# Kernel tuning notes

Hardware: AMD Instinct MI355X
Metric: run time of the kernel (lower is better)

The kernel has to match this reference:

```python
import jax, jax.numpy as jnp
import numpy as np
import math

B, S, N_EMBD, HEAD_SIZE = 32, 2048, 64, 64

def setup_inputs() -> dict:
    key = jax.random.key(0)
    k1, k2, k3, k4 = jax.random.split(key, 4)
    inputs = jax.random.normal(k1, (B, S, N_EMBD), dtype=jnp.float32)
    # nn.Linear(n_embd, head_size, bias=False) weights: shape (head_size, n_embd)
    scale = 1.0 / math.sqrt(N_EMBD)
    Wq = jax.random.normal(k2, (HEAD_SIZE, N_EMBD), dtype=jnp.float32) * scale
    Wk = jax.random.normal(k3, (HEAD_SIZE, N_EMBD), dtype=jnp.float32) * scale
    Wv = jax.random.normal(k4, (HEAD_SIZE, N_EMBD), dtype=jnp.float32) * scale
    return {"inputs": inputs, "Wq": Wq, "Wk": Wk, "Wv": Wv}

def reference(inputs, Wq, Wk, Wv):
    # q, k, v: [B, S, head_size]
    q = jnp.einsum('bse,he->bsh', inputs, Wq)
    k = jnp.einsum('bse,he->bsh', inputs, Wk)
    v = jnp.einsum('bse,he->bsh', inputs, Wv)
    scores = jnp.einsum('bqh,bkh->bqk', q, k) / jnp.sqrt(jnp.float32(HEAD_SIZE))
    # NOTE: the original torch code calls scores.masked_fill(...) out-of-place
    # and discards the result, so NO causal mask is actually applied.
    attention = jax.nn.softmax(scores, axis=-1)
    out = jnp.einsum('bqk,bkh->bqh', attention, v)  # [B, S, head_size]
    return out
```

## Files before the change

kernel.cpp:

```cpp
#include <hip/hip_runtime.h>


#define BATCH 32
#define SEQ   2048
#define HS    64
#define QSCALE 0.18033688011112042f
#define OTS   72
#define OPAD  20

typedef _Float16 f16x8 __attribute__((ext_vector_type(8)));
typedef _Float16 f16x4 __attribute__((ext_vector_type(4)));
typedef float    f32x4 __attribute__((ext_vector_type(4)));

__global__ __launch_bounds__(256) void prep_w(
    const float* __restrict__ Wq, const float* __restrict__ Wk,
    const float* __restrict__ Wv, _Float16* __restrict__ Wh)
{
    int i = blockIdx.x * 256 + threadIdx.x;
    int rep = i / 12288;
    int j = i - rep * 12288;
    const float* src = (j < 4096) ? Wq : ((j < 8192) ? Wk : Wv);
    float scale = (j < 4096) ? QSCALE : 1.0f;
    Wh[i] = (_Float16)(src[j & 4095] * scale);
}

__global__ __launch_bounds__(256) void proj_kernel(
    const float* __restrict__ x, const _Float16* __restrict__ Wh,
    _Float16* __restrict__ Qh, _Float16* __restrict__ Kh,
    _Float16* __restrict__ Vt)
{
    __shared__ __align__(16) _Float16 ot[64 * OTS];

    const int t    = threadIdx.x;
    const int w    = t >> 6;
    const int lane = t & 63;
    const int lo   = lane & 15;
    const int quad = lane >> 4;
    const long blk0 = (long)blockIdx.x * 64;
    const int  b    = (int)(blk0 / SEQ);
    const int  s0   = (int)(blk0 % SEQ);
    const long rw   = blk0 + w * 16;
    const _Float16* Wrep = Wh + (blockIdx.x & 7) * 12288;

    const float* xp = x + (rw + lo) * HS + quad * 8;
    float4 x0 = *(const float4*)xp;
    float4 x1 = *(const float4*)(xp + 4);
    float4 x2 = *(const float4*)(xp + 32);
    float4 x3 = *(const float4*)(xp + 36);
    f16x8 xb0, xb1;
    xb0[0]=(_Float16)x0.x; xb0[1]=(_Float16)x0.y; xb0[2]=(_Float16)x0.z; xb0[3]=(_Float16)x0.w;
    xb0[4]=(_Float16)x1.x; xb0[5]=(_Float16)x1.y; xb0[6]=(_Float16)x1.z; xb0[7]=(_Float16)x1.w;
    xb1[0]=(_Float16)x2.x; xb1[1]=(_Float16)x2.y; xb1[2]=(_Float16)x2.z; xb1[3]=(_Float16)x2.w;
    xb1[4]=(_Float16)x3.x; xb1[5]=(_Float16)x3.y; xb1[6]=(_Float16)x3.z; xb1[7]=(_Float16)x3.w;

#pragma unroll
    for (int m = 0; m < 3; ++m) {
        const _Float16* Wm = Wrep + m * 4096;
        f32x4 acc[4];
#pragma unroll
        for (int nt = 0; nt < 4; ++nt) { acc[nt][0]=0.f; acc[nt][1]=0.f; acc[nt][2]=0.f; acc[nt][3]=0.f; }
#pragma unroll
        for (int nt = 0; nt < 4; ++nt) {
            f16x8 wa0 = *(const f16x8*)(Wm + (nt * 16 + lo) * 64 + quad * 8);
            f16x8 wa1 = *(const f16x8*)(Wm + (nt * 16 + lo) * 64 + 32 + quad * 8);
            acc[nt] = __builtin_amdgcn_mfma_f32_16x16x32_f16(wa0, xb0, acc[nt], 0, 0, 0);
            acc[nt] = __builtin_amdgcn_mfma_f32_16x16x32_f16(wa1, xb1, acc[nt], 0, 0, 0);
        }
        if (m < 2) {
            _Float16* dst = (m == 0) ? Qh : Kh;
#pragma unroll
            for (int nt = 0; nt < 4; ++nt) {
                f16x4 pk;
                pk[0]=(_Float16)acc[nt][0]; pk[1]=(_Float16)acc[nt][1];
                pk[2]=(_Float16)acc[nt][2]; pk[3]=(_Float16)acc[nt][3];
                *(f16x4*)(dst + (rw + lo) * HS + nt * 16 + quad * 4) = pk;
            }
        } else {
#pragma unroll
            for (int nt = 0; nt < 4; ++nt)
#pragma unroll
                for (int r = 0; r < 4; ++r)
                    ot[(nt * 16 + quad * 4 + r) * OTS + w * 16 + lo] = (_Float16)acc[nt][r];
            __syncthreads();
            const int row = t >> 2, c = t & 3;
            f16x8 r0 = *(const f16x8*)(ot + row * OTS + c * 16);
            f16x8 r1 = *(const f16x8*)(ot + row * OTS + c * 16 + 8);
            _Float16* vd = Vt + ((long)b * HS + row) * SEQ + s0 + c * 16;
            *(f16x8*)vd       = r0;
            *(f16x8*)(vd + 8) = r1;
        }
    }
}

__global__ __launch_bounds__(256) void attn_kernel(
    const _Float16* __restrict__ Q, const _Float16* __restrict__ K,
    const _Float16* __restrict__ Vt, float* __restrict__ out)
{
    __shared__ __align__(16) _Float16 KV[2][8192];

    const int t    = threadIdx.x;
    const int w    = t >> 6;
    const int lane = t & 63;
    const int lo   = lane & 15;
    const int quad = lane >> 4;
    const int sr   = t >> 2, sc = t & 3;
    const int xr   = lo & 7;

    const int bid = blockIdx.x;
    const int b   = (bid & 7) | ((bid >> 8) << 3);
    const int qt  = (bid >> 3) & 31;
    const int q0  = qt * 64;
    const int qh  = w >> 1;
    const int kh  = w & 1;

    const _Float16* Qb = Q + ((long)b * SEQ + q0 + qh * 32) * HS;
    f16x8 qf[2][2];
#pragma unroll
    for (int q2 = 0; q2 < 2; ++q2) {
        qf[q2][0] = *(const f16x8*)(Qb + (q2 * 16 + lo) * HS + quad * 8);
        qf[q2][1] = *(const f16x8*)(Qb + (q2 * 16 + lo) * HS + 32 + quad * 8);
    }

    const _Float16* Kb = K  + (long)b * SEQ * HS;
    const _Float16* Vb = Vt + (long)b * HS * SEQ;

    const int pr  = (sr & 32) | ((sr & 4) << 2) | ((sr & 24) >> 1) | (sr & 3);
    const int kw0 = pr * 64 + (((2 * sc    ) ^ (pr & 7)) << 3);
    const int kw1 = pr * 64 + (((2 * sc + 1) ^ (pr & 7)) << 3);
    const int vw0 = 4096 + sr * 64 + (((2 * sc    ) ^ (sr & 7)) << 3);
    const int vw1 = 4096 + sr * 64 + (((2 * sc + 1) ^ (sr & 7)) << 3);

    const int kr0 = (kh * 32      + lo) * 64;
    const int kr1 = (kh * 32 + 16 + lo) * 64;
    const int g0  = ((quad    ) ^ xr) << 3;
    const int g1  = ((4 + quad) ^ xr) << 3;
    int voff[4];
#pragma unroll
    for (int ht = 0; ht < 4; ++ht)
        voff[ht] = 4096 + (ht * 16 + lo) * 64 + (((kh * 4 + quad) ^ xr) << 3);

    f32x4 o[2][4], ol[2];
#pragma unroll
    for (int q2 = 0; q2 < 2; ++q2) {
        ol[q2][0]=0.f; ol[q2][1]=0.f; ol[q2][2]=0.f; ol[q2][3]=0.f;
#pragma unroll
        for (int ht = 0; ht < 4; ++ht) { o[q2][ht][0]=0.f; o[q2][ht][1]=0.f; o[q2][ht][2]=0.f; o[q2][ht][3]=0.f; }
    }
    f32x4 zz; zz[0]=0.f; zz[1]=0.f; zz[2]=0.f; zz[3]=0.f;
    f16x8 ones;
#pragma unroll
    for (int j = 0; j < 8; ++j) ones[j] = (_Float16)1.0f;

    const int key0 = (qt & 31) << 6;
    f16x8 kfA = *(const f16x8*)(Kb + (long)(key0 + sr) * HS + sc * 16);
    f16x8 kfB = *(const f16x8*)(Kb + (long)(key0 + sr) * HS + sc * 16 + 8);
    f16x8 vfA = *(const f16x8*)(Vb + (long)sr * SEQ + key0 + sc * 16);
    f16x8 vfB = *(const f16x8*)(Vb + (long)sr * SEQ + key0 + sc * 16 + 8);

    for (int kt = 0; kt < 32; ++kt) {
        _Float16* Ksp = &KV[kt & 1][0];
        *(f16x8*)(Ksp + kw0) = kfA;
        *(f16x8*)(Ksp + kw1) = kfB;
        *(f16x8*)(Ksp + vw0) = vfA;
        *(f16x8*)(Ksp + vw1) = vfB;

        const int keyn = ((kt + 1 + qt) & 31) << 6;
        kfA = *(const f16x8*)(Kb + (long)(keyn + sr) * HS + sc * 16);
        kfB = *(const f16x8*)(Kb + (long)(keyn + sr) * HS + sc * 16 + 8);
        vfA = *(const f16x8*)(Vb + (long)sr * SEQ + keyn + sc * 16);
        vfB = *(const f16x8*)(Vb + (long)sr * SEQ + keyn + sc * 16 + 8);

        __syncthreads();

        f16x8 ka00 = *(const f16x8*)(Ksp + kr0 + g0);
        f16x8 ka01 = *(const f16x8*)(Ksp + kr0 + g1);
        f16x8 ka10 = *(const f16x8*)(Ksp + kr1 + g0);
        f16x8 ka11 = *(const f16x8*)(Ksp + kr1 + g1);

        f16x8 vbf[4];
#pragma unroll
        for (int ht = 0; ht < 4; ++ht)
            vbf[ht] = *(const f16x8*)(Ksp + voff[ht]);

#pragma unroll
        for (int q2 = 0; q2 < 2; ++q2) {
            f32x4 s0, s1;
            s0 = __builtin_amdgcn_mfma_f32_16x16x32_f16(ka00, qf[q2][0], zz, 0, 0, 0);
            s0 = __builtin_amdgcn_mfma_f32_16x16x32_f16(ka01, qf[q2][1], s0, 0, 0, 0);
            s1 = __builtin_amdgcn_mfma_f32_16x16x32_f16(ka10, qf[q2][0], zz, 0, 0, 0);
            s1 = __builtin_amdgcn_mfma_f32_16x16x32_f16(ka11, qf[q2][1], s1, 0, 0, 0);

            float e0 = __builtin_amdgcn_exp2f(s0[0]);
            float e1 = __builtin_amdgcn_exp2f(s0[1]);
            float e2 = __builtin_amdgcn_exp2f(s0[2]);
            float e3 = __builtin_amdgcn_exp2f(s0[3]);
            float e4 = __builtin_amdgcn_exp2f(s1[0]);
            float e5 = __builtin_amdgcn_exp2f(s1[1]);
            float e6 = __builtin_amdgcn_exp2f(s1[2]);
            float e7 = __builtin_amdgcn_exp2f(s1[3]);

            f16x8 pa;
            pa[0]=(_Float16)e0; pa[1]=(_Float16)e1; pa[2]=(_Float16)e2; pa[3]=(_Float16)e3;
            pa[4]=(_Float16)e4; pa[5]=(_Float16)e5; pa[6]=(_Float16)e6; pa[7]=(_Float16)e7;

            ol[q2] = __builtin_amdgcn_mfma_f32_16x16x32_f16(pa, ones, ol[q2], 0, 0, 0);
#pragma unroll
            for (int ht = 0; ht < 4; ++ht)
                o[q2][ht] = __builtin_amdgcn_mfma_f32_16x16x32_f16(pa, vbf[ht], o[q2][ht], 0, 0, 0);
        }
    }

    __syncthreads();
    float* obuf = (float*)&KV[0][0];
    float* lsm  = obuf + 4 * 32 * OPAD;

    if (lo == 0) {
#pragma unroll
        for (int q2 = 0; q2 < 2; ++q2)
#pragma unroll
            for (int r = 0; r < 4; ++r)
                lsm[w * 32 + q2 * 16 + quad * 4 + r] = ol[q2][r];
    }

    const int ql = w * 16 + (lane >> 2);
    const int hc = lane & 3;
    const int ra = (2 * (ql >> 5)) * 32 + (ql & 31);
    const int rb = (2 * (ql >> 5) + 1) * 32 + (ql & 31);
    float inv = 0.f;

    for (int ht = 0; ht < 4; ++ht) {
#pragma unroll
        for (int q2 = 0; q2 < 2; ++q2)
#pragma unroll
            for (int r = 0; r < 4; ++r)
                obuf[(w * 32 + q2 * 16 + quad * 4 + r) * OPAD + lo] = o[q2][ht][r];
        __syncthreads();
        if (ht == 0) inv = 1.0f / (lsm[ra] + lsm[rb]);
        f32x4 sum = *(const f32x4*)&obuf[ra * OPAD + hc * 4];
        sum = sum + *(const f32x4*)&obuf[rb * OPAD + hc * 4];
        sum = sum * inv;
        *(f32x4*)(out + ((long)b * SEQ + q0 + ql) * HS + ht * 16 + hc * 4) = sum;
        __syncthreads();
    }
}

extern "C" void kernel_launch(void* const* d_in, const int* in_sizes, int n_in,
                              void* d_out, int out_size, void* d_ws, size_t ws_size,
                              hipStream_t stream)
{
    const float* x  = (const float*)d_in[0];
    const float* Wq = (const float*)d_in[1];
    const float* Wk = (const float*)d_in[2];
    const float* Wv = (const float*)d_in[3];
    float* out = (float*)d_out;

    const size_t E = (size_t)BATCH * SEQ * HS;
    _Float16* Qh = (_Float16*)d_ws;
    _Float16* Kh = Qh + E;
    _Float16* Vt = Kh + E;
    _Float16* Wh = Vt + E;

    prep_w<<<384, 256, 0, stream>>>(Wq, Wk, Wv, Wh);
    proj_kernel<<<(BATCH * SEQ) / 64, 256, 0, stream>>>(x, Wh, Qh, Kh, Vt);
    attn_kernel<<<BATCH * (SEQ / 64), 256, 0, stream>>>(Qh, Kh, Vt, out);
}
```

Measured before the change: 141.7 us.

## Double attention query tile to 128 rows per block and simplify split-K merge

Each attention block now handles 128 queries instead of 64: every wave holds 64 query rows in registers and reuses each staged K/V tile across four 16-row groups. This halves the number of blocks and the total K/V global and LDS traffic per query. The epilogue is rewritten so one key-half wave group writes its partial output and row sums to shared memory and the other adds its own registers, normalizes and stores directly, replacing the four-pass loop with two barriers. In exchange, register pressure roughly doubles for accumulators and Q fragments, and there are fewer blocks (512) to spread across CUs.

```diff
diff --git a/kernel.cpp b/kernel.cpp
--- a/kernel.cpp
+++ b/kernel.cpp
@@ -6,7 +6,7 @@
 #define HS    64
 #define QSCALE 0.18033688011112042f
 #define OTS   72
-#define OPAD  20
+#define MSTR  68
 
 typedef _Float16 f16x8 __attribute__((ext_vector_type(8)));
 typedef _Float16 f16x4 __attribute__((ext_vector_type(4)));
@@ -96,7 +96,10 @@
     const _Float16* __restrict__ Q, const _Float16* __restrict__ K,
     const _Float16* __restrict__ Vt, float* __restrict__ out)
 {
-    __shared__ __align__(16) _Float16 KV[2][8192];
+    __shared__ __align__(16) char smem[35840];
+    _Float16* KVb  = (_Float16*)smem;
+    float*    obuf = (float*)smem;
+    float*    lbuf = obuf + 128 * MSTR;
 
     const int t    = threadIdx.x;
     const int w    = t >> 6;
@@ -107,16 +110,16 @@
     const int xr   = lo & 7;
 
     const int bid = blockIdx.x;
-    const int b   = (bid & 7) | ((bid >> 8) << 3);
-    const int qt  = (bid >> 3) & 31;
-    const int q0  = qt * 64;
+    const int b   = (bid & 7) | ((bid >> 7) << 3);
+    const int qt  = (bid >> 3) & 15;
+    const int q0  = qt * 128;
     const int qh  = w >> 1;
     const int kh  = w & 1;
 
-    const _Float16* Qb = Q + ((long)b * SEQ + q0 + qh * 32) * HS;
-    f16x8 qf[2][2];
-#pragma unroll
-    for (int q2 = 0; q2 < 2; ++q2) {
+    const _Float16* Qb = Q + ((long)b * SEQ + q0 + qh * 64) * HS;
+    f16x8 qf[4][2];
+#pragma unroll
+    for (int q2 = 0; q2 < 4; ++q2) {
         qf[q2][0] = *(const f16x8*)(Qb + (q2 * 16 + lo) * HS + quad * 8);
         qf[q2][1] = *(const f16x8*)(Qb + (q2 * 16 + lo) * HS + 32 + quad * 8);
     }
@@ -139,9 +142,9 @@
     for (int ht = 0; ht < 4; ++ht)
         voff[ht] = 4096 + (ht * 16 + lo) * 64 + (((kh * 4 + quad) ^ xr) << 3);
 
-    f32x4 o[2][4], ol[2];
-#pragma unroll
-    for (int q2 = 0; q2 < 2; ++q2) {
+    f32x4 o[4][4], ol[4];
+#pragma unroll
+    for (int q2 = 0; q2 < 4; ++q2) {
         ol[q2][0]=0.f; ol[q2][1]=0.f; ol[q2][2]=0.f; ol[q2][3]=0.f;
 #pragma unroll
         for (int ht = 0; ht < 4; ++ht) { o[q2][ht][0]=0.f; o[q2][ht][1]=0.f; o[q2][ht][2]=0.f; o[q2][ht][3]=0.f; }
@@ -151,20 +154,21 @@
 #pragma unroll
     for (int j = 0; j < 8; ++j) ones[j] = (_Float16)1.0f;
 
-    const int key0 = (qt & 31) << 6;
+    const int phase = qt << 1;
+    const int key0 = (phase & 31) << 6;
     f16x8 kfA = *(const f16x8*)(Kb + (long)(key0 + sr) * HS + sc * 16);
     f16x8 kfB = *(const f16x8*)(Kb + (long)(key0 + sr) * HS + sc * 16 + 8);
     f16x8 vfA = *(const f16x8*)(Vb + (long)sr * SEQ + key0 + sc * 16);
     f16x8 vfB = *(const f16x8*)(Vb + (long)sr * SEQ + key0 + sc * 16 + 8);
 
     for (int kt = 0; kt < 32; ++kt) {
-        _Float16* Ksp = &KV[kt & 1][0];
+        _Float16* Ksp = KVb + (kt & 1) * 8192;
         *(f16x8*)(Ksp + kw0) = kfA;
         *(f16x8*)(Ksp + kw1) = kfB;
         *(f16x8*)(Ksp + vw0) = vfA;
         *(f16x8*)(Ksp + vw1) = vfB;
 
-        const int keyn = ((kt + 1 + qt) & 31) << 6;
+        const int keyn = ((kt + 1 + phase) & 31) << 6;
         kfA = *(const f16x8*)(Kb + (long)(keyn + sr) * HS + sc * 16);
         kfB = *(const f16x8*)(Kb + (long)(keyn + sr) * HS + sc * 16 + 8);
         vfA = *(const f16x8*)(Vb + (long)sr * SEQ + keyn + sc * 16);
@@ -183,7 +187,7 @@
             vbf[ht] = *(const f16x8*)(Ksp + voff[ht]);
 
 #pragma unroll
-        for (int q2 = 0; q2 < 2; ++q2) {
+        for (int q2 = 0; q2 < 4; ++q2) {
             f32x4 s0, s1;
             s0 = __builtin_amdgcn_mfma_f32_16x16x32_f16(ka00, qf[q2][0], zz, 0, 0, 0);
             s0 = __builtin_amdgcn_mfma_f32_16x16x32_f16(ka01, qf[q2][1], s0, 0, 0, 0);
@@ -211,36 +215,38 @@
     }
 
     __syncthreads();
-    float* obuf = (float*)&KV[0][0];
-    float* lsm  = obuf + 4 * 32 * OPAD;
-
-    if (lo == 0) {
-#pragma unroll
-        for (int q2 = 0; q2 < 2; ++q2)
+    if (kh == 0) {
+#pragma unroll
+        for (int q2 = 0; q2 < 4; ++q2) {
+#pragma unroll
+            for (int ht = 0; ht < 4; ++ht)
+#pragma unroll
+                for (int r = 0; r < 4; ++r)
+                    obuf[(qh * 64 + q2 * 16 + quad * 4 + r) * MSTR + ht * 16 + lo] = o[q2][ht][r];
+            if (lo == 0) {
+#pragma unroll
+                for (int r = 0; r < 4; ++r)
+                    lbuf[qh * 64 + q2 * 16 + quad * 4 + r] = ol[q2][r];
+            }
+        }
+    }
+    __syncthreads();
+    if (kh == 1) {
+#pragma unroll
+        for (int q2 = 0; q2 < 4; ++q2) {
+            float linv[4];
 #pragma unroll
             for (int r = 0; r < 4; ++r)
-                lsm[w * 32 + q2 * 16 + quad * 4 + r] = ol[q2][r];
-    }
-
-    const int ql = w * 16 + (lane >> 2);
-    const int hc = lane & 3;
-    const int ra = (2 * (ql >> 5)) * 32 + (ql & 31);
-    const int rb = (2 * (ql >> 5) + 1) * 32 + (ql & 31);
-    float inv = 0.f;
-
-    for (int ht = 0; ht < 4; ++ht) {
-#pragma unroll
-        for (int q2 = 0; q2 < 2; ++q2)
-#pragma unroll
-            for (int r = 0; r < 4; ++r)
-                obuf[(w * 32 + q2 * 16 + quad * 4 + r) * OPAD + lo] = o[q2][ht][r];
-        __syncthreads();
-        if (ht == 0) inv = 1.0f / (lsm[ra] + lsm[rb]);
-        f32x4 sum = *(const f32x4*)&obuf[ra * OPAD + hc * 4];
-        sum = sum + *(const f32x4*)&obuf[rb * OPAD + hc * 4];
-        sum = sum * inv;
-        *(f32x4*)(out + ((long)b * SEQ + q0 + ql) * HS + ht * 16 + hc * 4) = sum;
-        __syncthreads();
+                linv[r] = 1.0f / (lbuf[qh * 64 + q2 * 16 + quad * 4 + r] + ol[q2][r]);
+#pragma unroll
+            for (int ht = 0; ht < 4; ++ht)
+#pragma unroll
+                for (int r = 0; r < 4; ++r) {
+                    const int row = qh * 64 + q2 * 16 + quad * 4 + r;
+                    float v = (obuf[row * MSTR + ht * 16 + lo] + o[q2][ht][r]) * linv[r];
+                    out[((long)b * SEQ + q0 + row) * HS + ht * 16 + lo] = v;
+                }
+        }
     }
 }
 
@@ -262,5 +268,5 @@
 
     prep_w<<<384, 256, 0, stream>>>(Wq, Wk, Wv, Wh);
     proj_kernel<<<(BATCH * SEQ) / 64, 256, 0, stream>>>(x, Wh, Qh, Kh, Vt);
-    attn_kernel<<<BATCH * (SEQ / 64), 256, 0, stream>>>(Qh, Kh, Vt, out);
-}
+    attn_kernel<<<BATCH * (SEQ / 128), 256, 0, stream>>>(Qh, Kh, Vt, out);
+}
```

New measurement: 136.7 us. 3.5% less time.
